# Kernel tuning notes

Hardware: AMD Instinct MI355X
Metric: run time of the kernel (lower is better)

Reference implementation:

```python
import jax, jax.numpy as jnp
import numpy as np

EMBED_DIM = 1024
NUM_HEADS = 16
HEAD_DIM = EMBED_DIM // NUM_HEADS


def setup_inputs() -> dict:
    key = jax.random.key(0)
    ks = jax.random.split(key, 5)
    scale = 1.0 / np.sqrt(EMBED_DIM)
    x = jax.random.normal(ks[0], (2, 2048, EMBED_DIM), dtype=jnp.float32)
    W_qkv = jax.random.uniform(ks[1], (EMBED_DIM, 3 * EMBED_DIM), jnp.float32, -scale, scale)
    b_qkv = jax.random.uniform(ks[2], (3 * EMBED_DIM,), jnp.float32, -scale, scale)
    W_out = jax.random.uniform(ks[3], (EMBED_DIM, EMBED_DIM), jnp.float32, -scale, scale)
    b_out = jax.random.uniform(ks[4], (EMBED_DIM,), jnp.float32, -scale, scale)
    return {"x": x, "W_qkv": W_qkv, "b_qkv": b_qkv, "W_out": W_out, "b_out": b_out}


def reference(x, W_qkv, b_qkv, W_out, b_out):
    B, T, C = x.shape
    H, D = NUM_HEADS, HEAD_DIM
    qkv = x @ W_qkv + b_qkv                       # [B,T,3C]
    q, k, v = jnp.split(qkv, 3, axis=-1)
    # [B,T,C] -> [B,H,T,D]
    q = q.reshape(B, T, H, D).transpose(0, 2, 1, 3)
    k = k.reshape(B, T, H, D).transpose(0, 2, 1, 3)
    v = v.reshape(B, T, H, D).transpose(0, 2, 1, 3)
    scores = jnp.einsum('bhqd,bhkd->bhqk', q, k) / np.sqrt(D)
    attn = jax.nn.softmax(scores, axis=-1)
    out = jnp.einsum('bhqk,bhkd->bhqd', attn, v)  # [B,H,T,D]
    out = out.transpose(0, 2, 1, 3).reshape(B, T, C)
    return out @ W_out + b_out
```

## Files before the change

kernel.cpp:

```cpp
#include <hip/hip_runtime.h>
#include <hip/hip_bf16.h>

#define TB 2048
#define CC 1024
#define HH 16
#define DD 64
#define MM 4096
#define N3 3072
#define KVB 128
#define NT (TB / KVB)

typedef __bf16 bf16x8 __attribute__((ext_vector_type(8)));
typedef float f32x4 __attribute__((ext_vector_type(4)));
typedef float f32x16 __attribute__((ext_vector_type(16)));
typedef unsigned short ushort8 __attribute__((ext_vector_type(8)));
typedef unsigned short u16;

#define QSCALE 0.180336880693612f

__device__ __forceinline__ u16 f2b(float f) {
    unsigned int x = __float_as_uint(f);
    x = (x + 0x7fffu + ((x >> 16) & 1u)) >> 16;
    return (u16)x;
}

__device__ __forceinline__ unsigned cvt_pk_bf16(float lo, float hi) {
    unsigned r;
    asm("v_cvt_pk_bf16_f32 %0, %1, %2" : "=v"(r) : "v"(lo), "v"(hi));
    return r;
}

__device__ __forceinline__ void gld16(const u16* g, u16* l) {
    __builtin_amdgcn_global_load_lds(
        (const __attribute__((address_space(1))) unsigned int*)g,
        (__attribute__((address_space(3))) unsigned int*)l, 16, 0, 0);
}

__global__ __launch_bounds__(256) void prep(const float* __restrict__ x,
                                            u16* __restrict__ xb,
                                            const float* __restrict__ wqkv,
                                            u16* __restrict__ wqkvT,
                                            const float* __restrict__ wout,
                                            u16* __restrict__ woutT) {
    __shared__ float tl[64][65];
    const int bx = blockIdx.x;
    const int tid = threadIdx.x;
    if (bx < 4096) {
        int i = (bx * 256 + tid) * 4;
        float4 v = *reinterpret_cast<const float4*>(x + i);
        union { u16 u[4]; uint2 v2; } r;
        r.u[0] = f2b(v.x); r.u[1] = f2b(v.y); r.u[2] = f2b(v.z); r.u[3] = f2b(v.w);
        *reinterpret_cast<uint2*>(xb + i) = r.v2;
        return;
    }
    const int idx = bx - 4096;
    const int nb = idx & 63, kb = idx >> 6;
    const float* in; u16* out; int N, n0;
    if (nb < 48) { in = wqkv; out = wqkvT; N = 3072; n0 = nb * 64; }
    else         { in = wout; out = woutT; N = 1024; n0 = (nb - 48) * 64; }
    const int k0 = kb * 64;
#pragma unroll
    for (int rep = 0; rep < 16; ++rep) {
        int id2 = rep * 256 + tid;
        int r = id2 >> 6, c = id2 & 63;
        tl[r][c] = in[(size_t)(k0 + r) * N + n0 + c];
    }
    __syncthreads();
#pragma unroll
    for (int rep = 0; rep < 16; ++rep) {
        int id2 = rep * 256 + tid;
        int r = id2 >> 6, c = id2 & 63;
        out[(size_t)(n0 + r) * 1024 + k0 + c] = f2b(tl[c][r]);
    }
}

__global__ __launch_bounds__(256) void gemm_qkv(const u16* __restrict__ xb,
                                                const u16* __restrict__ wT,
                                                const float* __restrict__ bias,
                                                u16* __restrict__ qg,
                                                u16* __restrict__ kg,
                                                u16* __restrict__ vtg) {
    __shared__ u16 smem[2 * 128 * 64];
    u16* As = smem;
    u16* Bs = smem + 128 * 64;
    const int id = blockIdx.y * 24 + blockIdx.x;
    const int xcd = id & 7, pos = id >> 3;
    const int xr = xcd >> 1, xc = xcd & 1;
    const int pr = pos / 12, pc = pos % 12;
    const int m0 = (xr * 8 + pr) * 128;
    const int n0 = (xc * 12 + pc) * 128;
    const int tid = threadIdx.x;
    const int w = tid >> 6, lane = tid & 63, lr = lane & 15, h = lane >> 4;
    const int wr = w >> 1, wc = w & 1;
    f32x4 acc[4][4] = {};

    for (int k0 = 0; k0 < 1024; k0 += 64) {
        __syncthreads();
#pragma unroll
        for (int j = 0; j < 4; ++j) {
            int L = j * 256 + tid;
            int r = L >> 3, c = L & 7;
            int csw = (c ^ (r & 7)) << 3;
            gld16(xb + (size_t)(m0 + r) * 1024 + k0 + csw, As + L * 8);
            gld16(wT + (size_t)(n0 + r) * 1024 + k0 + csw, Bs + L * 8);
        }
        __syncthreads();
#pragma unroll
        for (int kk = 0; kk < 2; ++kk) {
            bf16x8 a[4], b[4];
            int cc = kk * 4 + h;
#pragma unroll
            for (int m = 0; m < 4; ++m) {
                int R = wr * 64 + m * 16 + lr;
                a[m] = *reinterpret_cast<const bf16x8*>((const char*)As + R * 128 + ((cc ^ (R & 7)) << 4));
            }
#pragma unroll
            for (int n = 0; n < 4; ++n) {
                int R = wc * 64 + n * 16 + lr;
                b[n] = *reinterpret_cast<const bf16x8*>((const char*)Bs + R * 128 + ((cc ^ (R & 7)) << 4));
            }
#pragma unroll
            for (int m = 0; m < 4; ++m)
#pragma unroll
                for (int n = 0; n < 4; ++n)
                    acc[m][n] = __builtin_amdgcn_mfma_f32_16x16x32_bf16(a[m], b[n], acc[m][n], 0, 0, 0);
        }
    }

    const int nthird = n0 >> 10;
    const int b = m0 >> 11, t0 = m0 & 2047;
    if (nthird == 2) {
        __syncthreads();
#pragma unroll
        for (int n = 0; n < 4; ++n) {
            int nloc = wc * 64 + n * 16 + lr;
            unsigned xorv = (unsigned)(nloc & 15) << 4;
            float bv = bias[n0 + nloc];
#pragma unroll
            for (int m = 0; m < 4; ++m) {
                int mloc = wr * 64 + m * 16 + h * 4;
                int mp = (mloc & ~15) | (mloc & 3) | ((mloc & 4) << 1) | ((mloc & 8) >> 1);
                union { u16 u[4]; unsigned long long ll; } pk4;
#pragma unroll
                for (int reg = 0; reg < 4; ++reg)
                    pk4.u[reg] = f2b(acc[m][n][reg] + bv);
                *reinterpret_cast<unsigned long long*>(
                    (char*)smem + nloc * 256 + ((unsigned)(mp * 2) ^ xorv)) = pk4.ll;
            }
        }
        __syncthreads();
        const int c16 = tid & 15;
#pragma unroll
        for (int step = 0; step < 8; ++step) {
            int row = (tid >> 4) + step * 16;
            ushort8 vch = *reinterpret_cast<const ushort8*>(
                (const char*)smem + row * 256 + ((unsigned)((c16 ^ (row & 15)) << 4)));
            int c1 = (n0 + row) & 1023;
            int hh = c1 >> 6, dd = c1 & 63;
            *reinterpret_cast<ushort8*>(
                vtg + ((size_t)(b * HH + hh) * DD + dd) * TB + t0 + c16 * 8) = vch;
        }
    } else {
        const float qs = (nthird == 0) ? QSCALE : 1.0f;
        __syncthreads();
#pragma unroll
        for (int n = 0; n < 4; ++n) {
            int nloc = wc * 64 + n * 16 + lr;
            float bv = bias[n0 + nloc];
#pragma unroll
            for (int m = 0; m < 4; ++m) {
#pragma unroll
                for (int reg = 0; reg < 4; ++reg) {
                    int mloc = wr * 64 + m * 16 + h * 4 + reg;
                    *reinterpret_cast<u16*>((char*)smem + mloc * 256 +
                        ((unsigned)(nloc * 2) ^ ((unsigned)(mloc & 15) << 4)))
                        = f2b((acc[m][n][reg] + bv) * qs);
                }
            }
        }
        __syncthreads();
        u16* dst = (nthird == 0) ? qg : kg;
        const int c16 = tid & 15;
#pragma unroll
        for (int step = 0; step < 8; ++step) {
            int row = (tid >> 4) + step * 16;
            ushort8 vch = *reinterpret_cast<const ushort8*>(
                (const char*)smem + row * 256 + ((unsigned)((c16 ^ (row & 15)) << 4)));
            int colbase = c16 * 8;
            int c1 = (n0 + colbase) & 1023;
            int hh = c1 >> 6, dd = c1 & 63;
            *reinterpret_cast<ushort8*>(
                dst + ((size_t)(b * HH + hh) * TB + (t0 + row)) * DD + dd) = vch;
        }
    }
}

__global__ __launch_bounds__(256, 2) void attn(const u16* __restrict__ qg,
                                               const u16* __restrict__ kg,
                                               const u16* __restrict__ vtg,
                                               u16* __restrict__ ao) {
    __shared__ u16 Kt[2][KVB * 64];
    __shared__ u16 Vt[2][64 * KVB];
    const int bh = blockIdx.x;
    const int q0 = blockIdx.y * 128;
    const int tid = threadIdx.x, w = tid >> 6, lane = tid & 63;
    const int ln = lane & 31, H = lane >> 5;
    const u16* qb = qg + (size_t)bh * TB * DD;
    const u16* kb = kg + (size_t)bh * TB * DD;
    const u16* vb = vtg + (size_t)bh * DD * TB;

#define STAGE(buf, kp, vp) do {                                                         \
    _Pragma("unroll")                                                                   \
    for (int j = 0; j < 4; ++j) {                                                       \
        int L = j * 256 + tid;                                                          \
        int rk = L >> 3, ck = L & 7;                                                    \
        gld16((kp) + (size_t)rk * DD + ((ck ^ (rk & 7)) << 3), Kt[buf] + L * 8);        \
        int rv = L >> 4, cv = L & 15;                                                   \
        gld16((vp) + (size_t)rv * TB + ((cv ^ (rv & 15)) << 3), Vt[buf] + L * 8);       \
    } } while (0)

    bf16x8 bq[4];
#pragma unroll
    for (int dc = 0; dc < 4; ++dc)
        bq[dc] = *reinterpret_cast<const bf16x8*>(
            qb + (size_t)(q0 + w * 32 + ln) * DD + dc * 16 + H * 8);

    f32x16 o[2] = {};
    float m_r = -1e30f;
    float l_r = 0.f;
    f32x16 zero16 = {};

    auto tile_body = [&](const u16* ktc, const u16* vtc) {
        f32x16 s[4];
        __builtin_amdgcn_s_setprio(1);
#pragma unroll
        for (int kb4 = 0; kb4 < 4; ++kb4) {
            int R = kb4 * 32 + ln;
            const char* krow = (const char*)ktc + R * 128;
#pragma unroll
            for (int dc = 0; dc < 4; ++dc) {
                bf16x8 ak = *reinterpret_cast<const bf16x8*>(
                    krow + (((dc * 2 + H) ^ (R & 7)) << 4));
                s[kb4] = __builtin_amdgcn_mfma_f32_32x32x16_bf16(
                    ak, bq[dc], dc == 0 ? zero16 : s[kb4], 0, 0, 0);
            }
        }
        __builtin_amdgcn_s_setprio(0);

        float pm = s[0][0];
#pragma unroll
        for (int kb4 = 0; kb4 < 4; ++kb4) {
            float t0 = fmaxf(fmaxf(s[kb4][0], s[kb4][1]), fmaxf(s[kb4][2], s[kb4][3]));
            float t1 = fmaxf(fmaxf(s[kb4][4], s[kb4][5]), fmaxf(s[kb4][6], s[kb4][7]));
            float t2 = fmaxf(fmaxf(s[kb4][8], s[kb4][9]), fmaxf(s[kb4][10], s[kb4][11]));
            float t3 = fmaxf(fmaxf(s[kb4][12], s[kb4][13]), fmaxf(s[kb4][14], s[kb4][15]));
            pm = fmaxf(pm, fmaxf(fmaxf(t0, t1), fmaxf(t2, t3)));
        }
        pm = fmaxf(pm, __shfl_xor(pm, 32));

        if (!__all(pm - m_r <= 8.0f)) {
            float mn = fmaxf(m_r, pm);
            float fr = __builtin_amdgcn_exp2f(m_r - mn);
            m_r = mn;
            l_r *= fr;
#pragma unroll
            for (int ngd = 0; ngd < 2; ++ngd)
#pragma unroll
                for (int r = 0; r < 16; ++r)
                    o[ngd][r] *= fr;
        }

        float sum = 0.f;
#pragma unroll
        for (int kb4 = 0; kb4 < 4; ++kb4) {
            float ps = 0.f;
#pragma unroll
            for (int r = 0; r < 16; ++r) {
                s[kb4][r] = __builtin_amdgcn_exp2f(s[kb4][r] - m_r);
                ps += s[kb4][r];
            }
            sum += ps;
        }
        sum += __shfl_xor(sum, 32);
        l_r += sum;

        __builtin_amdgcn_s_setprio(1);
#pragma unroll
        for (int kb4 = 0; kb4 < 4; ++kb4) {
#pragma unroll
            for (int b1 = 0; b1 < 2; ++b1) {
                union { unsigned u[4]; bf16x8 v; } ap;
                ap.u[0] = cvt_pk_bf16(s[kb4][8 * b1 + 0], s[kb4][8 * b1 + 1]);
                ap.u[1] = cvt_pk_bf16(s[kb4][8 * b1 + 2], s[kb4][8 * b1 + 3]);
                ap.u[2] = cvt_pk_bf16(s[kb4][8 * b1 + 4], s[kb4][8 * b1 + 5]);
                ap.u[3] = cvt_pk_bf16(s[kb4][8 * b1 + 6], s[kb4][8 * b1 + 7]);
                int c = kb4 * 2 + b1;
#pragma unroll
                for (int ngd = 0; ngd < 2; ++ngd) {
                    int d = ngd * 32 + ln;
                    bf16x8 av = *reinterpret_cast<const bf16x8*>(
                        (const char*)vtc + d * 256 + (((c * 2 + H) ^ (d & 15)) << 4));
                    o[ngd] = __builtin_amdgcn_mfma_f32_32x32x16_bf16(av, ap.v, o[ngd], 0, 0, 0);
                }
            }
        }
        __builtin_amdgcn_s_setprio(0);
    };

    STAGE(0, kb, vb);
    const u16* kp = kb + KVB * DD;
    const u16* vp = vb + KVB;
    __syncthreads();

#pragma unroll 1
    for (int kt2 = 0; kt2 < NT / 2; ++kt2) {
        STAGE(1, kp, vp);
        kp += KVB * DD; vp += KVB;
        tile_body(Kt[0], Vt[0]);
        __syncthreads();
        if (kt2 < NT / 2 - 1) {
            STAGE(0, kp, vp);
            kp += KVB * DD; vp += KVB;
        }
        tile_body(Kt[1], Vt[1]);
        __syncthreads();
    }
#undef STAGE

    const float linv = 1.0f / l_r;
    const int b = bh >> 4, hh = bh & 15;
    const int q = q0 + w * 32 + ln;
    u16* aorow = ao + (size_t)(b * TB + q) * CC + hh * 64;
#pragma unroll
    for (int ngd = 0; ngd < 2; ++ngd) {
#pragma unroll
        for (int rg = 0; rg < 4; ++rg) {
            int dbase = ngd * 32 + 8 * rg + 4 * H;
            union { u16 u[4]; unsigned long long ll; } pk;
#pragma unroll
            for (int r2 = 0; r2 < 4; ++r2)
                pk.u[r2] = f2b(o[ngd][4 * rg + r2] * linv);
            *reinterpret_cast<unsigned long long*>(aorow + dbase) = pk.ll;
        }
    }
}

__global__ __launch_bounds__(256) void gemm_out(const u16* __restrict__ ao,
                                                const u16* __restrict__ wT,
                                                const float* __restrict__ bias,
                                                float* __restrict__ out) {
    __shared__ u16 As[64 * 64];
    __shared__ u16 Bs[128 * 64];
    const int id = blockIdx.y * 8 + blockIdx.x;
    const int xcd = id & 7, pos = id >> 3;
    const int xr = xcd >> 1, xc = xcd & 1;
    const int pr = pos >> 2, pc = pos & 3;
    const int m0 = (xr * 16 + pr) * 64;
    const int n0 = (xc * 4 + pc) * 128;
    const int tid = threadIdx.x;
    const int w = tid >> 6, lane = tid & 63, lr = lane & 15, h = lane >> 4;
    f32x4 acc[4][2] = {};

    for (int k0 = 0; k0 < 1024; k0 += 64) {
        __syncthreads();
#pragma unroll
        for (int j = 0; j < 2; ++j) {
            int L = j * 256 + tid;
            int r = L >> 3, c = L & 7;
            gld16(ao + (size_t)(m0 + r) * 1024 + k0 + ((c ^ (r & 7)) << 3), As + L * 8);
        }
#pragma unroll
        for (int j = 0; j < 4; ++j) {
            int L = j * 256 + tid;
            int r = L >> 3, c = L & 7;
            gld16(wT + (size_t)(n0 + r) * 1024 + k0 + ((c ^ (r & 7)) << 3), Bs + L * 8);
        }
        __syncthreads();
#pragma unroll
        for (int kk = 0; kk < 2; ++kk) {
            bf16x8 a[4], b[2];
            int cc = kk * 4 + h;
#pragma unroll
            for (int m = 0; m < 4; ++m) {
                int R = m * 16 + lr;
                a[m] = *reinterpret_cast<const bf16x8*>((const char*)As + R * 128 + ((cc ^ (R & 7)) << 4));
            }
#pragma unroll
            for (int n = 0; n < 2; ++n) {
                int R = w * 32 + n * 16 + lr;
                b[n] = *reinterpret_cast<const bf16x8*>((const char*)Bs + R * 128 + ((cc ^ (R & 7)) << 4));
            }
#pragma unroll
            for (int m = 0; m < 4; ++m)
#pragma unroll
                for (int n = 0; n < 2; ++n)
                    acc[m][n] = __builtin_amdgcn_mfma_f32_16x16x32_bf16(a[m], b[n], acc[m][n], 0, 0, 0);
        }
    }

#pragma unroll
    for (int n = 0; n < 2; ++n) {
        int ng = n0 + w * 32 + n * 16 + lr;
        float bv = bias[ng];
#pragma unroll
        for (int m = 0; m < 4; ++m) {
#pragma unroll
            for (int reg = 0; reg < 4; ++reg) {
                int mg = m0 + m * 16 + h * 4 + reg;
                out[(size_t)mg * 1024 + ng] = acc[m][n][reg] + bv;
            }
        }
    }
}

extern "C" void kernel_launch(void* const* d_in, const int* in_sizes, int n_in,
                              void* d_out, int out_size, void* d_ws, size_t ws_size,
                              hipStream_t stream) {
    const float* x     = (const float*)d_in[0];
    const float* W_qkv = (const float*)d_in[1];
    const float* b_qkv = (const float*)d_in[2];
    const float* W_out = (const float*)d_in[3];
    const float* b_out = (const float*)d_in[4];
    float* out = (float*)d_out;

    char* ws = (char*)d_ws;
    u16* xb    = (u16*)(ws);
    u16* wqkvT = (u16*)(ws + (size_t)( 8u << 20));
    u16* woutT = (u16*)(ws + (size_t)(14u << 20));
    u16* qg    = (u16*)(ws + (size_t)(16u << 20));
    u16* kg    = (u16*)(ws + (size_t)(24u << 20));
    u16* vtg   = (u16*)(ws + (size_t)(32u << 20));
    u16* ao    = xb;

    hipLaunchKernelGGL(prep, dim3(5120), dim3(256), 0, stream, x, xb, W_qkv, wqkvT, W_out, woutT);
    hipLaunchKernelGGL(gemm_qkv, dim3(24, 32), dim3(256), 0, stream, xb, wqkvT, b_qkv, qg, kg, vtg);
    hipLaunchKernelGGL(attn, dim3(32, 16), dim3(256), 0, stream, qg, kg, vtg, ao);
    hipLaunchKernelGGL(gemm_out, dim3(8, 64), dim3(256), 0, stream, ao, woutT, b_out, out);
}
```

Before: 117.9 us.

## Rewrite QKV GEMM with 256x256 tiles, double-buffered LDS and explicit wait scheduling

```diff
diff --git a/kernel.cpp b/kernel.cpp
--- a/kernel.cpp
+++ b/kernel.cpp
@@ -74,123 +74,184 @@
     }
 }
 
-__global__ __launch_bounds__(256) void gemm_qkv(const u16* __restrict__ xb,
-                                                const u16* __restrict__ wT,
-                                                const float* __restrict__ bias,
-                                                u16* __restrict__ qg,
-                                                u16* __restrict__ kg,
-                                                u16* __restrict__ vtg) {
-    __shared__ u16 smem[2 * 128 * 64];
-    u16* As = smem;
-    u16* Bs = smem + 128 * 64;
-    const int id = blockIdx.y * 24 + blockIdx.x;
+__global__ __launch_bounds__(512, 2) void gemm_qkv(const u16* __restrict__ xb,
+                                                   const u16* __restrict__ wT,
+                                                   const float* __restrict__ bias,
+                                                   u16* __restrict__ qg,
+                                                   u16* __restrict__ kg,
+                                                   u16* __restrict__ vtg) {
+    __shared__ u16 smem[65536];
+    u16* const A0 = smem;
+    u16* const B0 = smem + 16384;
+    u16* const A1 = smem + 32768;
+    u16* const B1 = smem + 49152;
+    const int id = blockIdx.y * 12 + blockIdx.x;
     const int xcd = id & 7, pos = id >> 3;
-    const int xr = xcd >> 1, xc = xcd & 1;
-    const int pr = pos / 12, pc = pos % 12;
-    const int m0 = (xr * 8 + pr) * 128;
-    const int n0 = (xc * 12 + pc) * 128;
+    const int m0 = ((xcd >> 1) * 4 + pos / 6) * 256;
+    const int n0 = ((xcd & 1) * 6 + pos % 6) * 256;
     const int tid = threadIdx.x;
     const int w = tid >> 6, lane = tid & 63, lr = lane & 15, h = lane >> 4;
-    const int wr = w >> 1, wc = w & 1;
-    f32x4 acc[4][4] = {};
-
-    for (int k0 = 0; k0 < 1024; k0 += 64) {
-        __syncthreads();
-#pragma unroll
-        for (int j = 0; j < 4; ++j) {
-            int L = j * 256 + tid;
-            int r = L >> 3, c = L & 7;
-            int csw = (c ^ (r & 7)) << 3;
-            gld16(xb + (size_t)(m0 + r) * 1024 + k0 + csw, As + L * 8);
-            gld16(wT + (size_t)(n0 + r) * 1024 + k0 + csw, Bs + L * 8);
-        }
-        __syncthreads();
-#pragma unroll
-        for (int kk = 0; kk < 2; ++kk) {
-            bf16x8 a[4], b[4];
-            int cc = kk * 4 + h;
-#pragma unroll
-            for (int m = 0; m < 4; ++m) {
-                int R = wr * 64 + m * 16 + lr;
-                a[m] = *reinterpret_cast<const bf16x8*>((const char*)As + R * 128 + ((cc ^ (R & 7)) << 4));
-            }
-#pragma unroll
-            for (int n = 0; n < 4; ++n) {
-                int R = wc * 64 + n * 16 + lr;
-                b[n] = *reinterpret_cast<const bf16x8*>((const char*)Bs + R * 128 + ((cc ^ (R & 7)) << 4));
-            }
-#pragma unroll
-            for (int m = 0; m < 4; ++m)
-#pragma unroll
-                for (int n = 0; n < 4; ++n)
-                    acc[m][n] = __builtin_amdgcn_mfma_f32_16x16x32_bf16(a[m], b[n], acc[m][n], 0, 0, 0);
-        }
-    }
+    const int wr = w >> 2, wc = w & 3;
+    f32x4 acc[8][4] = {};
+    bf16x8 bB[4][2];
+    bf16x8 a[2][2];
+
+#define STAGE_SIDE(dstb, srcp, rowbase, kt) do {                                      \
+    _Pragma("unroll")                                                                 \
+    for (int jj = 0; jj < 4; ++jj) {                                                  \
+        int L = jj * 512 + tid;                                                       \
+        int rr = L >> 3, c8 = L & 7;                                                  \
+        gld16((srcp) + (size_t)((rowbase) + rr) * 1024 + (kt) * 64                    \
+                  + ((c8 ^ (rr & 7)) << 3),                                           \
+              (dstb) + L * 8);                                                        \
+    } } while (0)
+#define DSREAD_B(PB) do {                                                             \
+    _Pragma("unroll")                                                                 \
+    for (int n = 0; n < 4; ++n) {                                                     \
+        int R = wc * 64 + n * 16 + lr;                                                \
+        const char* br = (const char*)(PB) + R * 128;                                 \
+        bB[n][0] = *reinterpret_cast<const bf16x8*>(br + ((h ^ (R & 7)) << 4));       \
+        bB[n][1] = *reinterpret_cast<const bf16x8*>(br + (((4 + h) ^ (R & 7)) << 4)); \
+    } } while (0)
+#define DSREAD_A(PA, mb) do {                                                         \
+    _Pragma("unroll")                                                                 \
+    for (int mi = 0; mi < 2; ++mi) {                                                  \
+        int R = wr * 128 + ((mb) + mi) * 16 + lr;                                     \
+        const char* ar = (const char*)(PA) + R * 128;                                 \
+        a[mi][0] = *reinterpret_cast<const bf16x8*>(ar + ((h ^ (R & 7)) << 4));       \
+        a[mi][1] = *reinterpret_cast<const bf16x8*>(ar + (((4 + h) ^ (R & 7)) << 4)); \
+    } } while (0)
+#define MFMAP(mb) do {                                                                \
+    _Pragma("unroll")                                                                 \
+    for (int mi = 0; mi < 2; ++mi)                                                    \
+        _Pragma("unroll")                                                             \
+        for (int n = 0; n < 4; ++n) {                                                 \
+            acc[(mb) + mi][n] = __builtin_amdgcn_mfma_f32_16x16x32_bf16(              \
+                a[mi][0], bB[n][0], acc[(mb) + mi][n], 0, 0, 0);                      \
+            acc[(mb) + mi][n] = __builtin_amdgcn_mfma_f32_16x16x32_bf16(              \
+                a[mi][1], bB[n][1], acc[(mb) + mi][n], 0, 0, 0);                      \
+        } } while (0)
+#define GBAR __builtin_amdgcn_s_barrier()
+#define VMC(n) asm volatile("s_waitcnt vmcnt(" #n ")" ::: "memory")
+#define LGK0 do { asm volatile("s_waitcnt lgkmcnt(0)" ::: "memory");                  \
+                  __builtin_amdgcn_sched_barrier(0); } while (0)
+#define PRI1 __builtin_amdgcn_s_setprio(1)
+#define PRI0 __builtin_amdgcn_s_setprio(0)
+
+    STAGE_SIDE(A0, xb, m0, 0);
+    STAGE_SIDE(B0, wT, n0, 0);
+
+#pragma unroll 1
+    for (int i = 0; i < 7; ++i) {
+        const int t1 = 2 * i + 1, t2 = 2 * i + 2;
+        STAGE_SIDE(A1, xb, m0, t1);
+        VMC(4); GBAR;
+        DSREAD_B(B0); DSREAD_A(A0, 0); LGK0;
+        PRI1; MFMAP(0); PRI0; GBAR;
+        STAGE_SIDE(B1, wT, n0, t1);
+        DSREAD_A(A0, 2); GBAR; LGK0; PRI1; MFMAP(2); PRI0; GBAR;
+        DSREAD_A(A0, 4); GBAR; LGK0; PRI1; MFMAP(4); PRI0; GBAR;
+        DSREAD_A(A0, 6); GBAR; LGK0; PRI1; MFMAP(6); PRI0; GBAR;
+        STAGE_SIDE(A0, xb, m0, t2);
+        VMC(4); GBAR;
+        DSREAD_B(B1); DSREAD_A(A1, 0); LGK0;
+        PRI1; MFMAP(0); PRI0; GBAR;
+        STAGE_SIDE(B0, wT, n0, t2);
+        DSREAD_A(A1, 2); GBAR; LGK0; PRI1; MFMAP(2); PRI0; GBAR;
+        DSREAD_A(A1, 4); GBAR; LGK0; PRI1; MFMAP(4); PRI0; GBAR;
+        DSREAD_A(A1, 6); GBAR; LGK0; PRI1; MFMAP(6); PRI0; GBAR;
+    }
+    STAGE_SIDE(A1, xb, m0, 15);
+    VMC(4); GBAR;
+    DSREAD_B(B0); DSREAD_A(A0, 0); LGK0;
+    PRI1; MFMAP(0); PRI0; GBAR;
+    STAGE_SIDE(B1, wT, n0, 15);
+    DSREAD_A(A0, 2); GBAR; LGK0; PRI1; MFMAP(2); PRI0; GBAR;
+    DSREAD_A(A0, 4); GBAR; LGK0; PRI1; MFMAP(4); PRI0; GBAR;
+    DSREAD_A(A0, 6); GBAR; LGK0; PRI1; MFMAP(6); PRI0; GBAR;
+    VMC(0); GBAR;
+    DSREAD_B(B1); DSREAD_A(A1, 0); LGK0;
+    PRI1; MFMAP(0); PRI0; GBAR;
+    DSREAD_A(A1, 2); GBAR; LGK0; PRI1; MFMAP(2); PRI0; GBAR;
+    DSREAD_A(A1, 4); GBAR; LGK0; PRI1; MFMAP(4); PRI0; GBAR;
+    DSREAD_A(A1, 6); GBAR; LGK0; PRI1; MFMAP(6); PRI0; GBAR;
+
+#undef STAGE_SIDE
+#undef DSREAD_B
+#undef DSREAD_A
+#undef MFMAP
+#undef GBAR
+#undef VMC
+#undef LGK0
+#undef PRI1
+#undef PRI0
 
     const int nthird = n0 >> 10;
     const int b = m0 >> 11, t0 = m0 & 2047;
+    float bv[4];
+#pragma unroll
+    for (int n = 0; n < 4; ++n)
+        bv[n] = bias[n0 + wc * 64 + n * 16 + lr];
+
+    __syncthreads();
     if (nthird == 2) {
-        __syncthreads();
 #pragma unroll
         for (int n = 0; n < 4; ++n) {
             int nloc = wc * 64 + n * 16 + lr;
-            unsigned xorv = (unsigned)(nloc & 15) << 4;
-            float bv = bias[n0 + nloc];
-#pragma unroll
-            for (int m = 0; m < 4; ++m) {
-                int mloc = wr * 64 + m * 16 + h * 4;
-                int mp = (mloc & ~15) | (mloc & 3) | ((mloc & 4) << 1) | ((mloc & 8) >> 1);
+#pragma unroll
+            for (int m = 0; m < 8; ++m) {
+                int mloc = wr * 128 + m * 16 + h * 4;
+                int mpb = (mloc & ~15) | ((mloc & 4) << 1) | ((mloc & 8) >> 1);
                 union { u16 u[4]; unsigned long long ll; } pk4;
 #pragma unroll
                 for (int reg = 0; reg < 4; ++reg)
-                    pk4.u[reg] = f2b(acc[m][n][reg] + bv);
+                    pk4.u[reg] = f2b(acc[m][n][reg] + bv[n]);
+                int slot = mpb >> 3;
                 *reinterpret_cast<unsigned long long*>(
-                    (char*)smem + nloc * 256 + ((unsigned)(mp * 2) ^ xorv)) = pk4.ll;
+                    (char*)smem + nloc * 512 + (((slot ^ (nloc & 31)) << 4) | ((mpb & 7) * 2))) = pk4.ll;
             }
         }
         __syncthreads();
-        const int c16 = tid & 15;
-#pragma unroll
-        for (int step = 0; step < 8; ++step) {
-            int row = (tid >> 4) + step * 16;
-            ushort8 vch = *reinterpret_cast<const ushort8*>(
-                (const char*)smem + row * 256 + ((unsigned)((c16 ^ (row & 15)) << 4)));
-            int c1 = (n0 + row) & 1023;
+#pragma unroll
+        for (int pass = 0; pass < 16; ++pass) {
+            int cid = pass * 512 + tid;
+            int r = cid >> 5, p = cid & 31;
+            ushort8 vch = *reinterpret_cast<const ushort8*>((const char*)smem + r * 512 + (p << 4));
+            int tb = p ^ (r & 31);
+            int c1 = (n0 & 1023) + r;
             int hh = c1 >> 6, dd = c1 & 63;
             *reinterpret_cast<ushort8*>(
-                vtg + ((size_t)(b * HH + hh) * DD + dd) * TB + t0 + c16 * 8) = vch;
+                vtg + ((size_t)(b * HH + hh) * DD + dd) * TB + t0 + tb * 8) = vch;
         }
     } else {
         const float qs = (nthird == 0) ? QSCALE : 1.0f;
-        __syncthreads();
-#pragma unroll
-        for (int n = 0; n < 4; ++n) {
-            int nloc = wc * 64 + n * 16 + lr;
-            float bv = bias[n0 + nloc];
-#pragma unroll
-            for (int m = 0; m < 4; ++m) {
+#pragma unroll
+        for (int m = 0; m < 8; ++m) {
+            int rb = wr * 128 + m * 16 + h * 4;
+#pragma unroll
+            for (int n = 0; n < 4; ++n) {
+                int c = wc * 64 + n * 16 + lr;
 #pragma unroll
                 for (int reg = 0; reg < 4; ++reg) {
-                    int mloc = wr * 64 + m * 16 + h * 4 + reg;
-                    *reinterpret_cast<u16*>((char*)smem + mloc * 256 +
-                        ((unsigned)(nloc * 2) ^ ((unsigned)(mloc & 15) << 4)))
-                        = f2b((acc[m][n][reg] + bv) * qs);
+                    int r = rb + reg;
+                    *reinterpret_cast<u16*>((char*)smem + r * 512 +
+                        ((((c >> 3) ^ (r & 31)) << 4) | ((c & 7) << 1)))
+                        = f2b((acc[m][n][reg] + bv[n]) * qs);
                 }
             }
         }
         __syncthreads();
         u16* dst = (nthird == 0) ? qg : kg;
-        const int c16 = tid & 15;
-#pragma unroll
-        for (int step = 0; step < 8; ++step) {
-            int row = (tid >> 4) + step * 16;
-            ushort8 vch = *reinterpret_cast<const ushort8*>(
-                (const char*)smem + row * 256 + ((unsigned)((c16 ^ (row & 15)) << 4)));
-            int colbase = c16 * 8;
-            int c1 = (n0 + colbase) & 1023;
+#pragma unroll
+        for (int pass = 0; pass < 16; ++pass) {
+            int cid = pass * 512 + tid;
+            int r = cid >> 5, p = cid & 31;
+            ushort8 vch = *reinterpret_cast<const ushort8*>((const char*)smem + r * 512 + (p << 4));
+            int cb = p ^ (r & 31);
+            int c1 = (n0 & 1023) + cb * 8;
             int hh = c1 >> 6, dd = c1 & 63;
             *reinterpret_cast<ushort8*>(
-                dst + ((size_t)(b * HH + hh) * TB + (t0 + row)) * DD + dd) = vch;
+                dst + ((size_t)(b * HH + hh) * TB + t0 + r) * DD + dd) = vch;
         }
     }
 }
@@ -433,7 +494,7 @@
     u16* ao    = xb;
 
     hipLaunchKernelGGL(prep, dim3(5120), dim3(256), 0, stream, x, xb, W_qkv, wqkvT, W_out, woutT);
-    hipLaunchKernelGGL(gemm_qkv, dim3(24, 32), dim3(256), 0, stream, xb, wqkvT, b_qkv, qg, kg, vtg);
+    hipLaunchKernelGGL(gemm_qkv, dim3(12, 16), dim3(512), 0, stream, xb, wqkvT, b_qkv, qg, kg, vtg);
     hipLaunchKernelGGL(attn, dim3(32, 16), dim3(256), 0, stream, qg, kg, vtg, ao);
     hipLaunchKernelGGL(gemm_out, dim3(8, 64), dim3(256), 0, stream, ao, woutT, b_out, out);
 }
```

Measured after the change: 110.1 us. -6.6%, faster.
